# Optimization experiments

Hardware: AMD Instinct MI355X
Metric: run time of the kernel (lower is better)

## Reference

```python
import jax, jax.numpy as jnp
import numpy as np

H, N, CH = 256, 64, 1

def _r2c(x):
    return x[..., 0] + 1j * x[..., 1]

def setup_inputs() -> dict:
    key = jax.random.key(0)
    kA, kB, kC, kdt = jax.random.split(key, 4)
    # Build a Hurwitz A (skew-Hermitian - 0.5*I) so dA = (I-dt/2 A)^-1 (I+dt/2 A) has spectral radius < 1
    M = jax.random.normal(kA, (H, N, N, 2), dtype=jnp.float32) / np.float32(np.sqrt(N))
    Mc = _r2c(M)
    Ac = 0.5 * (Mc - jnp.conjugate(jnp.swapaxes(Mc, -1, -2))) - 0.5 * jnp.eye(N, dtype=Mc.dtype)
    A = jnp.stack([Ac.real, Ac.imag], axis=-1)  # (H,N,N,2)
    B = jax.random.normal(kB, (H, N, 2), dtype=jnp.float32)
    C = jax.random.normal(kC, (CH, H, N, 2), dtype=jnp.float32)
    # log_dt uniform in [log(1e-3), log(1e-1)], shape (H,1) per bilinear docstring
    log_dt = jax.random.uniform(kdt, (H, 1), dtype=jnp.float32,
                                minval=np.float32(np.log(1e-3)), maxval=np.float32(np.log(1e-1)))
    return {"A": A, "B": B, "C": C, "log_dt": log_dt, "L": 2048}

def _bilinear(dt, Ac, Bc):
    # dt: (H,1), Ac: (H,N,N) complex, Bc: (H,N) complex
    n = Ac.shape[-1]
    I = jnp.eye(n, dtype=Ac.dtype)
    half = (dt.astype(Ac.real.dtype) / 2)[:, None]  # (H,1,1)
    A_back = I - half * Ac
    A_fwd = I + half * Ac
    dB = dt.astype(Ac.dtype) * jnp.linalg.solve(A_back, Bc[..., None])[..., 0]  # (H,N)
    dA = jnp.linalg.solve(A_back, A_fwd)  # (H,N,N)
    return dA, dB

def _krylov(L, dA, dB):
    # x[..., l] = dA^l dB via squaring-doubling, matches S4 krylov math
    x = dB[..., None]  # (H,N,1)
    A_ = dA
    while x.shape[-1] < L:
        x = jnp.concatenate([x, jnp.einsum('hnm,hml->hnl', A_, x)], axis=-1)
        A_ = A_ @ A_
    return x[..., :L]

def reference(A, B, C, log_dt, L):
    Ac, Bc, Cc = _r2c(A), _r2c(B), _r2c(C)
    dt = jnp.exp(log_dt)  # (H,1)
    dA, dB = _bilinear(dt, Ac, Bc)
    x = _krylov(L, dA, dB)  # (H,N,L) complex
    # k[c,h,l] = sum_n C[c,h,n] * (dA^l dB)[h,n]; torch .float() on complex keeps real part
    k = jnp.einsum('chn,hnl->chl', Cc, x).real.astype(jnp.float32)
    return k
```

## Files before the change

### kernel.cpp

```cpp
#include <hip/hip_runtime.h>
#include <math.h>

#define NH   256
#define NN   64
#define LSEQ 2048
#define SDW  68
#define NTH  1024

typedef __attribute__((ext_vector_type(8))) short short8;
typedef __attribute__((ext_vector_type(4))) float float4_t;

#define MFMA(a,b,c) __builtin_amdgcn_mfma_f32_16x16x32_bf16((a),(b),(c),0,0,0)
#define PERM_HI 0x07060302u
#define PERM_LO 0x05040100u

static __device__ __forceinline__ unsigned pack2(float v) {
    unsigned hv = __float_as_uint(v) & 0xffff0000u;
    float lo = v - __uint_as_float(hv);
    return __builtin_amdgcn_perm(hv, __float_as_uint(lo), PERM_HI);
}
static __device__ __forceinline__ float unpack2(unsigned w) {
    return __uint_as_float(w & 0xffff0000u) + __uint_as_float(w << 16);
}

static __device__ __forceinline__ void frag_vals(const unsigned* e, short8& hi, short8& lo) {
    unsigned lb[8];
#pragma unroll
    for (int m = 0; m < 8; ++m) {
        unsigned hv = e[m] & 0xffff0000u;
        lb[m] = __float_as_uint(__uint_as_float(e[m]) - __uint_as_float(hv));
    }
    union { short8 s; unsigned u[4]; } H, L;
#pragma unroll
    for (int m = 0; m < 4; ++m) {
        H.u[m] = __builtin_amdgcn_perm(e[2*m+1],  e[2*m],  PERM_HI);
        L.u[m] = __builtin_amdgcn_perm(lb[2*m+1], lb[2*m], PERM_HI);
    }
    hi = H.s; lo = L.s;
}
static __device__ __forceinline__ void frag_f32(const float* p, short8& hi, short8& lo) {
    const uint4* q = (const uint4*)p;
    uint4 d0 = q[0], d1 = q[1];
    unsigned e[8] = {d0.x, d0.y, d0.z, d0.w, d1.x, d1.y, d1.z, d1.w};
    frag_vals(e, hi, lo);
}
static __device__ __forceinline__ void frag_packed(const unsigned* p, short8& hi, short8& lo) {
    const uint4* q = (const uint4*)p;
    uint4 d0 = q[0], d1 = q[1];
    unsigned e[8] = {d0.x, d0.y, d0.z, d0.w, d1.x, d1.y, d1.z, d1.w};
    union { short8 s; unsigned u[4]; } H, L;
#pragma unroll
    for (int m = 0; m < 4; ++m) {
        H.u[m] = __builtin_amdgcn_perm(e[2*m+1], e[2*m], PERM_HI);
        L.u[m] = __builtin_amdgcn_perm(e[2*m+1], e[2*m], PERM_LO);
    }
    hi = H.s; lo = L.s;
}
static __device__ __forceinline__ short8 neg8(short8 v) {
    union { short8 s; int i[4]; } u; u.s = v;
#pragma unroll
    for (int m = 0; m < 4; ++m) u.i[m] ^= 0x80008000;
    return u.s;
}

template<bool AP, bool BP, bool IMAG>
static __device__ __forceinline__ void cmm_tile(
    const void* Ar_, const void* Ai_, const void* Br_, const void* Bi_,
    int arow, int bcol, int fq, float4_t& accR, float4_t& accI)
{
#pragma unroll
    for (int ks = 0; ks < 2; ++ks) {
        const int k0 = ks*32 + fq*8;
        short8 Arh, Arl, Aih, Ail, Brh, Brl, Bih, Bil;
        if (AP) {
            frag_packed((const unsigned*)Ar_ + arow*SDW + k0, Arh, Arl);
            frag_packed((const unsigned*)Ai_ + arow*SDW + k0, Aih, Ail);
        } else {
            frag_f32((const float*)Ar_ + arow*SDW + k0, Arh, Arl);
            frag_f32((const float*)Ai_ + arow*SDW + k0, Aih, Ail);
        }
        if (BP) {
            frag_packed((const unsigned*)Br_ + bcol*SDW + k0, Brh, Brl);
            frag_packed((const unsigned*)Bi_ + bcol*SDW + k0, Bih, Bil);
        } else {
            frag_f32((const float*)Br_ + bcol*SDW + k0, Brh, Brl);
            frag_f32((const float*)Bi_ + bcol*SDW + k0, Bih, Bil);
        }
        short8 nAih = neg8(Aih), nAil = neg8(Ail);
        accR = MFMA(Arh, Brh, accR); accR = MFMA(Arh, Brl, accR); accR = MFMA(Arl, Brh, accR);
        accR = MFMA(nAih, Bih, accR); accR = MFMA(nAih, Bil, accR); accR = MFMA(nAil, Bih, accR);
        if (IMAG) {
            accI = MFMA(Arh, Bih, accI); accI = MFMA(Arh, Bil, accI); accI = MFMA(Arl, Bih, accI);
            accI = MFMA(Aih, Brh, accI); accI = MFMA(Aih, Brl, accI); accI = MFMA(Ail, Brh, accI);
        }
    }
}

__global__ __launch_bounds__(NTH, 4) void ssm_kernel(
    const float* __restrict__ Ag,
    const float* __restrict__ Bg,
    const float* __restrict__ Cg,
    const float* __restrict__ LogDt,
    float* __restrict__ outp)
{
    __shared__ __align__(16) unsigned char lds[130688];
    unsigned* XRr = (unsigned*)(lds +      0);
    unsigned* XRi = (unsigned*)(lds +  17408);
    unsigned* XTr = (unsigned*)(lds +  34816);
    unsigned* XTi = (unsigned*)(lds +  52224);
    float*    Xfr = (float*)(lds +  69632);
    float*    Xfi = (float*)(lds +  87040);
    unsigned* U0u = (unsigned*)Xfr;
    unsigned* U1u = (unsigned*)Xfi;
    float*    Grf = (float*)(lds + 104448);
    float*    Gif = (float*)(lds + 113152);
    float*    Kof = (float*)(lds + 121856);
    float*    bvr = (float*)(lds + 130176);
    float*    bvi = (float*)(lds + 130432);

    const int t    = threadIdx.x;
    const int lane = t & 63;
    const int wv   = t >> 6;
    const int ti   = wv >> 2, tj = wv & 3;
    const int fm   = lane & 15, fq = lane >> 4;
    const int h    = blockIdx.x;

    const float dt  = expf(LogDt[h]);
    const float hdt = 0.5f * dt;

    const float2* A2 = (const float2*)(Ag + (size_t)h * NN * NN * 2);

#pragma unroll
    for (int e = 0; e < 4; ++e) {
        int idx = t + e*NTH;
        int i = idx >> 6, j = idx & 63;
        float2 a = A2[idx];
        unsigned pr = pack2((i == j ? 1.0f : 0.0f) + hdt * a.x);
        unsigned pi = pack2(hdt * a.y);
        XRr[i*SDW + j] = pr; XRi[i*SDW + j] = pi;
        XTr[j*SDW + i] = pr; XTi[j*SDW + i] = pi;
    }
    if (t < NN) {
        float2 bv = ((const float2*)Bg)[h*NN + t];
        float2 cv = ((const float2*)Cg)[h*NN + t];
        bvr[t] = bv.x; bvi[t] = bv.y;
        Grf[t] = cv.x; Gif[t] = cv.y;
    }
    __syncthreads();

    const int arow = ti*16 + fm;
    const int bcol = tj*16 + fm;

#pragma unroll 1
    for (int step = 0; step < 2; ++step) {
        float4_t aR = {0,0,0,0}, aI = {0,0,0,0};
#pragma unroll
        for (int ks = 0; ks < 2; ++ks) {
            const int k0 = ks*32 + fq*8;
            unsigned vr[8], vi[8];
#pragma unroll
            for (int j = 0; j < 8; ++j) {
                float2 a = A2[arow*NN + k0 + j];
                vr[j] = __float_as_uint((arow == k0 + j ? 1.0f : 0.0f) - hdt * a.x);
                vi[j] = __float_as_uint(-hdt * a.y);
            }
            short8 Arh, Arl, Aih, Ail, Brh, Brl, Bih, Bil;
            frag_vals(vr, Arh, Arl);
            frag_vals(vi, Aih, Ail);
            frag_packed(XTr + bcol*SDW + k0, Brh, Brl);
            frag_packed(XTi + bcol*SDW + k0, Bih, Bil);
            short8 nAih = neg8(Aih), nAil = neg8(Ail);
            aR = MFMA(Arh, Brh, aR); aR = MFMA(Arh, Brl, aR); aR = MFMA(Arl, Brh, aR);
            aR = MFMA(nAih, Bih, aR); aR = MFMA(nAih, Bil, aR); aR = MFMA(nAil, Bih, aR);
            aI = MFMA(Arh, Bih, aI); aI = MFMA(Arh, Bil, aI); aI = MFMA(Arl, Bih, aI);
            aI = MFMA(Aih, Brh, aI); aI = MFMA(Aih, Brl, aI); aI = MFMA(Ail, Brh, aI);
        }
#pragma unroll
        for (int r = 0; r < 4; ++r) {
            int row = ti*16 + fq*4 + r;
            U0u[bcol*SDW + row] = pack2((row == bcol ? 2.0f : 0.0f) - aR[r]);
            U1u[bcol*SDW + row] = pack2(-aI[r]);
        }
        __syncthreads();
        float4_t bR = {0,0,0,0}, bI = {0,0,0,0};
        cmm_tile<true, true, true>(XRr, XRi, U0u, U1u, arow, bcol, fq, bR, bI);
        __syncthreads();
#pragma unroll
        for (int r = 0; r < 4; ++r) {
            int row = ti*16 + fq*4 + r;
            unsigned pr = pack2(bR[r]), pi = pack2(bI[r]);
            XRr[row*SDW + bcol] = pr; XRi[row*SDW + bcol] = pi;
            XTr[bcol*SDW + row] = pr; XTi[bcol*SDW + row] = pi;
        }
        __syncthreads();
    }

    {
        int n = t >> 4, part = t & 15;
        float ar = 0.f, ai = 0.f;
#pragma unroll
        for (int qq = 0; qq < 4; ++qq) {
            int k = part + 16*qq;
            float mr = unpack2(XRr[n*SDW + k]), mi = unpack2(XRi[n*SDW + k]);
            ar += mr*bvr[k] - mi*bvi[k];
            ai += mr*bvi[k] + mi*bvr[k];
        }
#pragma unroll
        for (int off = 8; off; off >>= 1) { ar += __shfl_xor(ar, off); ai += __shfl_xor(ai, off); }
        if (part == 0) { Xfr[n] = dt*ar; Xfi[n] = dt*ai; }
    }
    __syncthreads();

#pragma unroll
    for (int e = 0; e < 4; ++e) {
        int idx = t + e*NTH;
        int i = idx >> 6, j = idx & 63;
        float vr = 2.0f*unpack2(XRr[i*SDW + j]) - (i == j ? 1.0f : 0.0f);
        float vi = 2.0f*unpack2(XRi[i*SDW + j]);
        unsigned pr = pack2(vr), pi = pack2(vi);
        XRr[i*SDW + j] = pr; XRi[i*SDW + j] = pi;
        XTr[j*SDW + i] = pr; XTi[j*SDW + i] = pi;
    }
    __syncthreads();

#pragma unroll 1
    for (int s = 1; s <= 11; ++s) {
        if (s <= 6) {
            const int C = 1 << (s-1);
            const int nT = (s == 6) ? 8 : 4;
            if (wv < nT) {
                const int rt = wv >> 2, ct = wv & 3;
                float4_t aR = {0,0,0,0}, aI = {0,0,0,0};
                cmm_tile<false, true, true>(Xfr, Xfi, XRr, XRi, rt*16 + fm, ct*16 + fm, fq, aR, aI);
#pragma unroll
                for (int r = 0; r < 4; ++r) {
                    int row = rt*16 + fq*4 + r;
                    Xfr[(C+row)*SDW + ct*16 + fm] = aR[r];
                    Xfi[(C+row)*SDW + ct*16 + fm] = aI[r];
                }
            }
        } else {
            const int C = 1 << (s-7);
            if (wv < 4) {
                float4_t aR = {0,0,0,0}, aI = {0,0,0,0};
                cmm_tile<false, true, true>(Grf, Gif, XTr, XTi, fm, wv*16 + fm, fq, aR, aI);
#pragma unroll
                for (int r = 0; r < 4; ++r) {
                    int row = fq*4 + r;
                    Grf[(C+row)*SDW + wv*16 + fm] = aR[r];
                    Gif[(C+row)*SDW + wv*16 + fm] = aI[r];
                }
            } else if (s == 11 && wv < 8) {
                int jo = wv - 4;
                float4_t aR = {0,0,0,0}, dummy = {0,0,0,0};
                cmm_tile<false, false, false>(Grf, Gif, Xfr, Xfi, fm, jo*16 + fm, fq, aR, dummy);
#pragma unroll
                for (int r = 0; r < 4; ++r)
                    Kof[(fq*4 + r)*65 + jo*16 + fm] = aR[r];
            }
        }
        if (s <= 10) {
            float4_t sR = {0,0,0,0}, sI = {0,0,0,0};
            cmm_tile<true, true, true>(XRr, XRi, XTr, XTi, arow, bcol, fq, sR, sI);
            __syncthreads();
#pragma unroll
            for (int r = 0; r < 4; ++r) {
                int row = ti*16 + fq*4 + r;
                unsigned pr = pack2(sR[r]), pi = pack2(sI[r]);
                XRr[row*SDW + bcol] = pr; XRi[row*SDW + bcol] = pi;
                XTr[bcol*SDW + row] = pr; XTi[bcol*SDW + row] = pi;
            }
            __syncthreads();
        } else {
            __syncthreads();
        }
    }

    if (wv < 4) {
        float4_t aR = {0,0,0,0}, dummy = {0,0,0,0};
        cmm_tile<false, false, false>(Grf, Gif, Xfr, Xfi, 16 + fm, wv*16 + fm, fq, aR, dummy);
#pragma unroll
        for (int r = 0; r < 4; ++r)
            Kof[(16 + fq*4 + r)*65 + wv*16 + fm] = aR[r];
    }
    __syncthreads();

    {
        int row = t >> 5, col = (t & 31) * 2;
        float2 v = { Kof[row*65 + col], Kof[row*65 + col + 1] };
        ((float2*)(outp + (size_t)h * LSEQ))[t] = v;
    }
}

extern "C" void kernel_launch(void* const* d_in, const int* in_sizes, int n_in,
                              void* d_out, int out_size, void* d_ws, size_t ws_size,
                              hipStream_t stream) {
    const float* A  = (const float*)d_in[0];
    const float* B  = (const float*)d_in[1];
    const float* C  = (const float*)d_in[2];
    const float* ld = (const float*)d_in[3];
    float* out = (float*)d_out;
    ssm_kernel<<<dim3(NH), dim3(NTH), 0, stream>>>(A, B, C, ld, out);
}
```

Measured before the change: 102.1 us.

## Halve block size and register-block complex matmuls into 2x2 tiles per wave

```diff
diff --git a/kernel.cpp b/kernel.cpp
--- a/kernel.cpp
+++ b/kernel.cpp
@@ -5,7 +5,7 @@
 #define NN   64
 #define LSEQ 2048
 #define SDW  68
-#define NTH  1024
+#define NTH  512
 
 typedef __attribute__((ext_vector_type(8))) short short8;
 typedef __attribute__((ext_vector_type(4))) float float4_t;
@@ -63,40 +63,61 @@
     return u.s;
 }
 
-template<bool AP, bool BP, bool IMAG>
-static __device__ __forceinline__ void cmm_tile(
+template<int AG, bool AP, bool BP, bool IMAG>
+static __device__ __forceinline__ void cmm_block(
     const void* Ar_, const void* Ai_, const void* Br_, const void* Bi_,
-    int arow, int bcol, int fq, float4_t& accR, float4_t& accI)
+    int arow0, int bcol0, int fm, int fq,
+    float4_t (&accR)[AG][2], float4_t (&accI)[AG][2])
 {
 #pragma unroll
     for (int ks = 0; ks < 2; ++ks) {
         const int k0 = ks*32 + fq*8;
-        short8 Arh, Arl, Aih, Ail, Brh, Brl, Bih, Bil;
-        if (AP) {
-            frag_packed((const unsigned*)Ar_ + arow*SDW + k0, Arh, Arl);
-            frag_packed((const unsigned*)Ai_ + arow*SDW + k0, Aih, Ail);
-        } else {
-            frag_f32((const float*)Ar_ + arow*SDW + k0, Arh, Arl);
-            frag_f32((const float*)Ai_ + arow*SDW + k0, Aih, Ail);
-        }
-        if (BP) {
-            frag_packed((const unsigned*)Br_ + bcol*SDW + k0, Brh, Brl);
-            frag_packed((const unsigned*)Bi_ + bcol*SDW + k0, Bih, Bil);
-        } else {
-            frag_f32((const float*)Br_ + bcol*SDW + k0, Brh, Brl);
-            frag_f32((const float*)Bi_ + bcol*SDW + k0, Bih, Bil);
-        }
-        short8 nAih = neg8(Aih), nAil = neg8(Ail);
-        accR = MFMA(Arh, Brh, accR); accR = MFMA(Arh, Brl, accR); accR = MFMA(Arl, Brh, accR);
-        accR = MFMA(nAih, Bih, accR); accR = MFMA(nAih, Bil, accR); accR = MFMA(nAil, Bih, accR);
-        if (IMAG) {
-            accI = MFMA(Arh, Bih, accI); accI = MFMA(Arh, Bil, accI); accI = MFMA(Arl, Bih, accI);
-            accI = MFMA(Aih, Brh, accI); accI = MFMA(Aih, Brl, accI); accI = MFMA(Ail, Brh, accI);
-        }
-    }
-}
-
-__global__ __launch_bounds__(NTH, 4) void ssm_kernel(
+        short8 Arh[AG], Arl[AG], Aih[AG], Ail[AG];
+#pragma unroll
+        for (int g = 0; g < AG; ++g) {
+            const int row = arow0 + g*16 + fm;
+            if (AP) {
+                frag_packed((const unsigned*)Ar_ + row*SDW + k0, Arh[g], Arl[g]);
+                frag_packed((const unsigned*)Ai_ + row*SDW + k0, Aih[g], Ail[g]);
+            } else {
+                frag_f32((const float*)Ar_ + row*SDW + k0, Arh[g], Arl[g]);
+                frag_f32((const float*)Ai_ + row*SDW + k0, Aih[g], Ail[g]);
+            }
+        }
+#pragma unroll
+        for (int bg = 0; bg < 2; ++bg) {
+            const int col = bcol0 + bg*16 + fm;
+            short8 Brh, Brl, Bih, Bil;
+            if (BP) {
+                frag_packed((const unsigned*)Br_ + col*SDW + k0, Brh, Brl);
+                frag_packed((const unsigned*)Bi_ + col*SDW + k0, Bih, Bil);
+            } else {
+                frag_f32((const float*)Br_ + col*SDW + k0, Brh, Brl);
+                frag_f32((const float*)Bi_ + col*SDW + k0, Bih, Bil);
+            }
+            short8 nBih = neg8(Bih), nBil = neg8(Bil);
+#pragma unroll
+            for (int g = 0; g < AG; ++g) {
+                accR[g][bg] = MFMA(Arh[g], Brh,  accR[g][bg]);
+                accR[g][bg] = MFMA(Arh[g], Brl,  accR[g][bg]);
+                accR[g][bg] = MFMA(Arl[g], Brh,  accR[g][bg]);
+                accR[g][bg] = MFMA(Aih[g], nBih, accR[g][bg]);
+                accR[g][bg] = MFMA(Aih[g], nBil, accR[g][bg]);
+                accR[g][bg] = MFMA(Ail[g], nBih, accR[g][bg]);
+                if (IMAG) {
+                    accI[g][bg] = MFMA(Arh[g], Bih, accI[g][bg]);
+                    accI[g][bg] = MFMA(Arh[g], Bil, accI[g][bg]);
+                    accI[g][bg] = MFMA(Arl[g], Bih, accI[g][bg]);
+                    accI[g][bg] = MFMA(Aih[g], Brh, accI[g][bg]);
+                    accI[g][bg] = MFMA(Aih[g], Brl, accI[g][bg]);
+                    accI[g][bg] = MFMA(Ail[g], Brh, accI[g][bg]);
+                }
+            }
+        }
+    }
+}
+
+__global__ __launch_bounds__(NTH) void ssm_kernel(
     const float* __restrict__ Ag,
     const float* __restrict__ Bg,
     const float* __restrict__ Cg,
@@ -121,7 +142,6 @@
     const int t    = threadIdx.x;
     const int lane = t & 63;
     const int wv   = t >> 6;
-    const int ti   = wv >> 2, tj = wv & 3;
     const int fm   = lane & 15, fq = lane >> 4;
     const int h    = blockIdx.x;
 
@@ -129,9 +149,10 @@
     const float hdt = 0.5f * dt;
 
     const float2* A2 = (const float2*)(Ag + (size_t)h * NN * NN * 2);
-
-#pragma unroll
-    for (int e = 0; e < 4; ++e) {
+    const float4_t z4 = {0.f, 0.f, 0.f, 0.f};
+
+#pragma unroll
+    for (int e = 0; e < 8; ++e) {
         int idx = t + e*NTH;
         int i = idx >> 6, j = idx & 63;
         float2 a = A2[idx];
@@ -148,71 +169,95 @@
     }
     __syncthreads();
 
-    const int arow = ti*16 + fm;
-    const int bcol = tj*16 + fm;
-
 #pragma unroll 1
     for (int step = 0; step < 2; ++step) {
-        float4_t aR = {0,0,0,0}, aI = {0,0,0,0};
-#pragma unroll
-        for (int ks = 0; ks < 2; ++ks) {
-            const int k0 = ks*32 + fq*8;
-            unsigned vr[8], vi[8];
-#pragma unroll
-            for (int j = 0; j < 8; ++j) {
-                float2 a = A2[arow*NN + k0 + j];
-                vr[j] = __float_as_uint((arow == k0 + j ? 1.0f : 0.0f) - hdt * a.x);
-                vi[j] = __float_as_uint(-hdt * a.y);
-            }
-            short8 Arh, Arl, Aih, Ail, Brh, Brl, Bih, Bil;
-            frag_vals(vr, Arh, Arl);
-            frag_vals(vi, Aih, Ail);
-            frag_packed(XTr + bcol*SDW + k0, Brh, Brl);
-            frag_packed(XTi + bcol*SDW + k0, Bih, Bil);
-            short8 nAih = neg8(Aih), nAil = neg8(Ail);
-            aR = MFMA(Arh, Brh, aR); aR = MFMA(Arh, Brl, aR); aR = MFMA(Arl, Brh, aR);
-            aR = MFMA(nAih, Bih, aR); aR = MFMA(nAih, Bil, aR); aR = MFMA(nAil, Bih, aR);
-            aI = MFMA(Arh, Bih, aI); aI = MFMA(Arh, Bil, aI); aI = MFMA(Arl, Bih, aI);
-            aI = MFMA(Aih, Brh, aI); aI = MFMA(Aih, Brl, aI); aI = MFMA(Ail, Brh, aI);
-        }
-#pragma unroll
-        for (int r = 0; r < 4; ++r) {
-            int row = ti*16 + fq*4 + r;
-            U0u[bcol*SDW + row] = pack2((row == bcol ? 2.0f : 0.0f) - aR[r]);
-            U1u[bcol*SDW + row] = pack2(-aI[r]);
-        }
-        __syncthreads();
-        float4_t bR = {0,0,0,0}, bI = {0,0,0,0};
-        cmm_tile<true, true, true>(XRr, XRi, U0u, U1u, arow, bcol, fq, bR, bI);
-        __syncthreads();
-#pragma unroll
-        for (int r = 0; r < 4; ++r) {
-            int row = ti*16 + fq*4 + r;
-            unsigned pr = pack2(bR[r]), pi = pack2(bI[r]);
-            XRr[row*SDW + bcol] = pr; XRi[row*SDW + bcol] = pi;
-            XTr[bcol*SDW + row] = pr; XTi[bcol*SDW + row] = pi;
+        {
+            const int arow0 = (wv >> 1) * 16;
+            const int bcol0 = (wv & 1) * 32;
+            float4_t aR[2], aI[2];
+            aR[0] = z4; aR[1] = z4; aI[0] = z4; aI[1] = z4;
+#pragma unroll
+            for (int ks = 0; ks < 2; ++ks) {
+                const int k0 = ks*32 + fq*8;
+                const int row = arow0 + fm;
+                unsigned vr[8], vi[8];
+#pragma unroll
+                for (int j = 0; j < 8; ++j) {
+                    float2 a = A2[row*NN + k0 + j];
+                    vr[j] = __float_as_uint((row == k0 + j ? 1.0f : 0.0f) - hdt * a.x);
+                    vi[j] = __float_as_uint(-hdt * a.y);
+                }
+                short8 Arh, Arl, Aih, Ail;
+                frag_vals(vr, Arh, Arl);
+                frag_vals(vi, Aih, Ail);
+#pragma unroll
+                for (int bg = 0; bg < 2; ++bg) {
+                    const int col = bcol0 + bg*16 + fm;
+                    short8 Brh, Brl, Bih, Bil;
+                    frag_packed(XTr + col*SDW + k0, Brh, Brl);
+                    frag_packed(XTi + col*SDW + k0, Bih, Bil);
+                    short8 nBih = neg8(Bih), nBil = neg8(Bil);
+                    aR[bg] = MFMA(Arh, Brh,  aR[bg]); aR[bg] = MFMA(Arh, Brl,  aR[bg]);
+                    aR[bg] = MFMA(Arl, Brh,  aR[bg]); aR[bg] = MFMA(Aih, nBih, aR[bg]);
+                    aR[bg] = MFMA(Aih, nBil, aR[bg]); aR[bg] = MFMA(Ail, nBih, aR[bg]);
+                    aI[bg] = MFMA(Arh, Bih,  aI[bg]); aI[bg] = MFMA(Arh, Bil,  aI[bg]);
+                    aI[bg] = MFMA(Arl, Bih,  aI[bg]); aI[bg] = MFMA(Aih, Brh,  aI[bg]);
+                    aI[bg] = MFMA(Aih, Brl,  aI[bg]); aI[bg] = MFMA(Ail, Brh,  aI[bg]);
+                }
+            }
+#pragma unroll
+            for (int bg = 0; bg < 2; ++bg)
+#pragma unroll
+                for (int r = 0; r < 4; ++r) {
+                    int row = arow0 + fq*4 + r;
+                    int col = bcol0 + bg*16 + fm;
+                    U0u[col*SDW + row] = pack2((row == col ? 2.0f : 0.0f) - aR[bg][r]);
+                    U1u[col*SDW + row] = pack2(-aI[bg][r]);
+                }
+        }
+        __syncthreads();
+        float4_t bR[2][2], bI[2][2];
+        bR[0][0]=z4; bR[0][1]=z4; bR[1][0]=z4; bR[1][1]=z4;
+        bI[0][0]=z4; bI[0][1]=z4; bI[1][0]=z4; bI[1][1]=z4;
+        if (wv < 4)
+            cmm_block<2, true, true, true>(XRr, XRi, U0u, U1u,
+                                           (wv>>1)*32, (wv&1)*32, fm, fq, bR, bI);
+        __syncthreads();
+        if (wv < 4) {
+#pragma unroll
+            for (int g = 0; g < 2; ++g)
+#pragma unroll
+                for (int bg = 0; bg < 2; ++bg)
+#pragma unroll
+                    for (int r = 0; r < 4; ++r) {
+                        int row = (wv>>1)*32 + g*16 + fq*4 + r;
+                        int col = (wv&1)*32 + bg*16 + fm;
+                        unsigned pr = pack2(bR[g][bg][r]), pi = pack2(bI[g][bg][r]);
+                        XRr[row*SDW + col] = pr; XRi[row*SDW + col] = pi;
+                        XTr[col*SDW + row] = pr; XTi[col*SDW + row] = pi;
+                    }
         }
         __syncthreads();
     }
 
     {
-        int n = t >> 4, part = t & 15;
+        int n = t >> 3, part = t & 7;
         float ar = 0.f, ai = 0.f;
 #pragma unroll
-        for (int qq = 0; qq < 4; ++qq) {
-            int k = part + 16*qq;
+        for (int qq = 0; qq < 8; ++qq) {
+            int k = part + 8*qq;
             float mr = unpack2(XRr[n*SDW + k]), mi = unpack2(XRi[n*SDW + k]);
             ar += mr*bvr[k] - mi*bvi[k];
             ai += mr*bvi[k] + mi*bvr[k];
         }
 #pragma unroll
-        for (int off = 8; off; off >>= 1) { ar += __shfl_xor(ar, off); ai += __shfl_xor(ai, off); }
+        for (int off = 4; off; off >>= 1) { ar += __shfl_xor(ar, off); ai += __shfl_xor(ai, off); }
         if (part == 0) { Xfr[n] = dt*ar; Xfi[n] = dt*ai; }
     }
     __syncthreads();
 
 #pragma unroll
-    for (int e = 0; e < 4; ++e) {
+    for (int e = 0; e < 8; ++e) {
         int idx = t + e*NTH;
         int i = idx >> 6, j = idx & 63;
         float vr = 2.0f*unpack2(XRr[i*SDW + j]) - (i == j ? 1.0f : 0.0f);
@@ -225,70 +270,116 @@
 
 #pragma unroll 1
     for (int s = 1; s <= 11; ++s) {
+        const bool dosq = (s <= 10);
+        float4_t sR[2][2], sI[2][2];
+        sR[0][0]=z4; sR[0][1]=z4; sR[1][0]=z4; sR[1][1]=z4;
+        sI[0][0]=z4; sI[0][1]=z4; sI[1][0]=z4; sI[1][1]=z4;
+        if (wv < 4 && dosq)
+            cmm_block<2, true, true, true>(XRr, XRi, XTr, XTi,
+                                           (wv>>1)*32, (wv&1)*32, fm, fq, sR, sI);
+        float4_t p1R[1][2], p1I[1][2];
+        p1R[0][0]=z4; p1R[0][1]=z4; p1I[0][0]=z4; p1I[0][1]=z4;
+        float4_t p2R[2][2], p2I[2][2];
+        p2R[0][0]=z4; p2R[0][1]=z4; p2R[1][0]=z4; p2R[1][1]=z4;
+        p2I[0][0]=z4; p2I[0][1]=z4; p2I[1][0]=z4; p2I[1][1]=z4;
+        int C;
         if (s <= 6) {
-            const int C = 1 << (s-1);
-            const int nT = (s == 6) ? 8 : 4;
-            if (wv < nT) {
-                const int rt = wv >> 2, ct = wv & 3;
-                float4_t aR = {0,0,0,0}, aI = {0,0,0,0};
-                cmm_tile<false, true, true>(Xfr, Xfi, XRr, XRi, rt*16 + fm, ct*16 + fm, fq, aR, aI);
-#pragma unroll
-                for (int r = 0; r < 4; ++r) {
-                    int row = rt*16 + fq*4 + r;
-                    Xfr[(C+row)*SDW + ct*16 + fm] = aR[r];
-                    Xfi[(C+row)*SDW + ct*16 + fm] = aI[r];
-                }
+            C = 1 << (s-1);
+            if (wv == 4 || wv == 5) {
+                if (s == 6)
+                    cmm_block<2, false, true, true>(Xfr, Xfi, XRr, XRi,
+                                                    0, (wv-4)*32, fm, fq, p2R, p2I);
+                else
+                    cmm_block<1, false, true, true>(Xfr, Xfi, XRr, XRi,
+                                                    0, (wv-4)*32, fm, fq, p1R, p1I);
             }
         } else {
-            const int C = 1 << (s-7);
-            if (wv < 4) {
-                float4_t aR = {0,0,0,0}, aI = {0,0,0,0};
-                cmm_tile<false, true, true>(Grf, Gif, XTr, XTi, fm, wv*16 + fm, fq, aR, aI);
-#pragma unroll
-                for (int r = 0; r < 4; ++r) {
-                    int row = fq*4 + r;
-                    Grf[(C+row)*SDW + wv*16 + fm] = aR[r];
-                    Gif[(C+row)*SDW + wv*16 + fm] = aI[r];
-                }
-            } else if (s == 11 && wv < 8) {
-                int jo = wv - 4;
-                float4_t aR = {0,0,0,0}, dummy = {0,0,0,0};
-                cmm_tile<false, false, false>(Grf, Gif, Xfr, Xfi, fm, jo*16 + fm, fq, aR, dummy);
+            C = 1 << (s-7);
+            if (wv == 4 || wv == 5)
+                cmm_block<1, false, true, true>(Grf, Gif, XTr, XTi,
+                                                0, (wv-4)*32, fm, fq, p1R, p1I);
+            if (s == 11 && (wv == 6 || wv == 7))
+                cmm_block<1, false, false, false>(Grf, Gif, Xfr, Xfi,
+                                                  0, (wv-6)*32, fm, fq, p1R, p1I);
+        }
+        if (wv == 4 || wv == 5) {
+            const int cb = (wv-4)*32;
+            if (s == 6) {
+#pragma unroll
+                for (int g = 0; g < 2; ++g)
+#pragma unroll
+                    for (int bg = 0; bg < 2; ++bg)
+#pragma unroll
+                        for (int r = 0; r < 4; ++r) {
+                            int row = 32 + g*16 + fq*4 + r;
+                            int col = cb + bg*16 + fm;
+                            Xfr[row*SDW + col] = p2R[g][bg][r];
+                            Xfi[row*SDW + col] = p2I[g][bg][r];
+                        }
+            } else if (s <= 5) {
+#pragma unroll
+                for (int bg = 0; bg < 2; ++bg)
+#pragma unroll
+                    for (int r = 0; r < 4; ++r) {
+                        int row = C + fq*4 + r;
+                        int col = cb + bg*16 + fm;
+                        Xfr[row*SDW + col] = p1R[0][bg][r];
+                        Xfi[row*SDW + col] = p1I[0][bg][r];
+                    }
+            } else {
+#pragma unroll
+                for (int bg = 0; bg < 2; ++bg)
+#pragma unroll
+                    for (int r = 0; r < 4; ++r) {
+                        int row = C + fq*4 + r;
+                        int col = cb + bg*16 + fm;
+                        Grf[row*SDW + col] = p1R[0][bg][r];
+                        Gif[row*SDW + col] = p1I[0][bg][r];
+                    }
+            }
+        }
+        if (s == 11 && (wv == 6 || wv == 7)) {
+#pragma unroll
+            for (int bg = 0; bg < 2; ++bg)
 #pragma unroll
                 for (int r = 0; r < 4; ++r)
-                    Kof[(fq*4 + r)*65 + jo*16 + fm] = aR[r];
-            }
-        }
-        if (s <= 10) {
-            float4_t sR = {0,0,0,0}, sI = {0,0,0,0};
-            cmm_tile<true, true, true>(XRr, XRi, XTr, XTi, arow, bcol, fq, sR, sI);
-            __syncthreads();
-#pragma unroll
-            for (int r = 0; r < 4; ++r) {
-                int row = ti*16 + fq*4 + r;
-                unsigned pr = pack2(sR[r]), pi = pack2(sI[r]);
-                XRr[row*SDW + bcol] = pr; XRi[row*SDW + bcol] = pi;
-                XTr[bcol*SDW + row] = pr; XTi[bcol*SDW + row] = pi;
-            }
-            __syncthreads();
-        } else {
-            __syncthreads();
-        }
-    }
-
-    if (wv < 4) {
-        float4_t aR = {0,0,0,0}, dummy = {0,0,0,0};
-        cmm_tile<false, false, false>(Grf, Gif, Xfr, Xfi, 16 + fm, wv*16 + fm, fq, aR, dummy);
-#pragma unroll
-        for (int r = 0; r < 4; ++r)
-            Kof[(16 + fq*4 + r)*65 + wv*16 + fm] = aR[r];
+                    Kof[(fq*4 + r)*65 + (wv-6)*32 + bg*16 + fm] = p1R[0][bg][r];
+        }
+        __syncthreads();
+        if (wv < 4 && dosq) {
+#pragma unroll
+            for (int g = 0; g < 2; ++g)
+#pragma unroll
+                for (int bg = 0; bg < 2; ++bg)
+#pragma unroll
+                    for (int r = 0; r < 4; ++r) {
+                        int row = (wv>>1)*32 + g*16 + fq*4 + r;
+                        int col = (wv&1)*32 + bg*16 + fm;
+                        unsigned pr = pack2(sR[g][bg][r]), pi = pack2(sI[g][bg][r]);
+                        XRr[row*SDW + col] = pr; XRi[row*SDW + col] = pi;
+                        XTr[col*SDW + row] = pr; XTi[col*SDW + row] = pi;
+                    }
+        }
+        __syncthreads();
+    }
+
+    if (wv < 2) {
+        float4_t kR[1][2], kI[1][2];
+        kR[0][0]=z4; kR[0][1]=z4; kI[0][0]=z4; kI[0][1]=z4;
+        cmm_block<1, false, false, false>(Grf, Gif, Xfr, Xfi, 16, wv*32, fm, fq, kR, kI);
+#pragma unroll
+        for (int bg = 0; bg < 2; ++bg)
+#pragma unroll
+            for (int r = 0; r < 4; ++r)
+                Kof[(16 + fq*4 + r)*65 + wv*32 + bg*16 + fm] = kR[0][bg][r];
     }
     __syncthreads();
 
     {
-        int row = t >> 5, col = (t & 31) * 2;
-        float2 v = { Kof[row*65 + col], Kof[row*65 + col + 1] };
-        ((float2*)(outp + (size_t)h * LSEQ))[t] = v;
+        int row = t >> 4, col = (t & 15) * 4;
+        const float4_t* src = (const float4_t*)(Kof + row*65 + col);
+        float4_t v = *src;
+        ((float4*)(outp + (size_t)h * LSEQ))[t] = make_float4(v[0], v[1], v[2], v[3]);
     }
 }
 
```

Result: slower. 105.6 us (+3.5%).

## Replace resolvent Newton steps with polynomial iteration and shorten squaring chain

Applied to the files above, without the earlier changes.

```diff
diff --git a/kernel.cpp b/kernel.cpp
--- a/kernel.cpp
+++ b/kernel.cpp
@@ -129,6 +129,7 @@
     const float hdt = 0.5f * dt;
 
     const float2* A2 = (const float2*)(Ag + (size_t)h * NN * NN * 2);
+    const float4_t z4 = {0.f, 0.f, 0.f, 0.f};
 
 #pragma unroll
     for (int e = 0; e < 4; ++e) {
@@ -151,9 +152,8 @@
     const int arow = ti*16 + fm;
     const int bcol = tj*16 + fm;
 
-#pragma unroll 1
-    for (int step = 0; step < 2; ++step) {
-        float4_t aR = {0,0,0,0}, aI = {0,0,0,0};
+    {
+        float4_t aR = z4, aI = z4;
 #pragma unroll
         for (int ks = 0; ks < 2; ++ks) {
             const int k0 = ks*32 + fq*8;
@@ -176,24 +176,62 @@
             aI = MFMA(Aih, Brh, aI); aI = MFMA(Aih, Brl, aI); aI = MFMA(Ail, Brh, aI);
         }
 #pragma unroll
+        for (int rp = 0; rp < 2; ++rp) {
+            int row0 = ti*16 + fq*4 + rp*2;
+            uint2 wr; wr.x = pack2(aR[rp*2]); wr.y = pack2(aR[rp*2+1]);
+            uint2 wi; wi.x = pack2(aI[rp*2]); wi.y = pack2(aI[rp*2+1]);
+            *(uint2*)(U0u + bcol*SDW + row0) = wr;
+            *(uint2*)(U1u + bcol*SDW + row0) = wi;
+        }
+    }
+    __syncthreads();
+
+    {
+        float4_t aR = z4, aI = z4;
+        cmm_tile<true, true, true>(XRr, XRi, U0u, U1u, arow, bcol, fq, aR, aI);
+        __syncthreads();
+#pragma unroll
         for (int r = 0; r < 4; ++r) {
             int row = ti*16 + fq*4 + r;
-            U0u[bcol*SDW + row] = pack2((row == bcol ? 2.0f : 0.0f) - aR[r]);
-            U1u[bcol*SDW + row] = pack2(-aI[r]);
-        }
-        __syncthreads();
-        float4_t bR = {0,0,0,0}, bI = {0,0,0,0};
-        cmm_tile<true, true, true>(XRr, XRi, U0u, U1u, arow, bcol, fq, bR, bI);
-        __syncthreads();
+            XRr[row*SDW + bcol] = pack2(aR[r]);
+            XRi[row*SDW + bcol] = pack2(aI[r]);
+        }
+    }
+    __syncthreads();
+
+    {
+        float4_t aR = z4, aI = z4;
+        cmm_tile<true, true, true>(XRr, XRi, U0u, U1u, arow, bcol, fq, aR, aI);
+        float o_r[4], o_i[4];
 #pragma unroll
         for (int r = 0; r < 4; ++r) {
             int row = ti*16 + fq*4 + r;
-            unsigned pr = pack2(bR[r]), pi = pack2(bI[r]);
-            XRr[row*SDW + bcol] = pr; XRi[row*SDW + bcol] = pi;
-            XTr[bcol*SDW + row] = pr; XTi[bcol*SDW + row] = pi;
-        }
-        __syncthreads();
-    }
+            float2 a = A2[row*NN + bcol];
+            float x1r = (row == bcol ? 1.0f : 0.0f) + hdt * a.x;
+            float x1i = hdt * a.y;
+            float vvr = unpack2(XRr[row*SDW + bcol]);
+            float vvi = unpack2(XRi[row*SDW + bcol]);
+            o_r[r] = 3.0f*x1r - 3.0f*vvr + aR[r];
+            o_i[r] = 3.0f*x1i - 3.0f*vvi + aI[r];
+        }
+        __syncthreads();
+        unsigned pr[4], pi[4];
+#pragma unroll
+        for (int r = 0; r < 4; ++r) {
+            int row = ti*16 + fq*4 + r;
+            pr[r] = pack2(o_r[r]); pi[r] = pack2(o_i[r]);
+            XRr[row*SDW + bcol] = pr[r]; XRi[row*SDW + bcol] = pi[r];
+        }
+#pragma unroll
+        for (int rp = 0; rp < 2; ++rp) {
+            int row0 = ti*16 + fq*4 + rp*2;
+            uint2 wr; wr.x = pr[rp*2]; wr.y = pr[rp*2+1];
+            uint2 wi; wi.x = pi[rp*2]; wi.y = pi[rp*2+1];
+            *(uint2*)(XTr + bcol*SDW + row0) = wr;
+            *(uint2*)(XTi + bcol*SDW + row0) = wi;
+        }
+    }
+    __syncthreads();
 
     {
         int n = t >> 4, part = t & 15;
@@ -224,13 +262,13 @@
     __syncthreads();
 
 #pragma unroll 1
-    for (int s = 1; s <= 11; ++s) {
+    for (int s = 1; s <= 9; ++s) {
         if (s <= 6) {
             const int C = 1 << (s-1);
             const int nT = (s == 6) ? 8 : 4;
             if (wv < nT) {
                 const int rt = wv >> 2, ct = wv & 3;
-                float4_t aR = {0,0,0,0}, aI = {0,0,0,0};
+                float4_t aR = z4, aI = z4;
                 cmm_tile<false, true, true>(Xfr, Xfi, XRr, XRi, rt*16 + fm, ct*16 + fm, fq, aR, aI);
 #pragma unroll
                 for (int r = 0; r < 4; ++r) {
@@ -242,7 +280,7 @@
         } else {
             const int C = 1 << (s-7);
             if (wv < 4) {
-                float4_t aR = {0,0,0,0}, aI = {0,0,0,0};
+                float4_t aR = z4, aI = z4;
                 cmm_tile<false, true, true>(Grf, Gif, XTr, XTi, fm, wv*16 + fm, fq, aR, aI);
 #pragma unroll
                 for (int r = 0; r < 4; ++r) {
@@ -250,40 +288,56 @@
                     Grf[(C+row)*SDW + wv*16 + fm] = aR[r];
                     Gif[(C+row)*SDW + wv*16 + fm] = aI[r];
                 }
-            } else if (s == 11 && wv < 8) {
-                int jo = wv - 4;
-                float4_t aR = {0,0,0,0}, dummy = {0,0,0,0};
-                cmm_tile<false, false, false>(Grf, Gif, Xfr, Xfi, fm, jo*16 + fm, fq, aR, dummy);
+            }
+        }
+        float4_t sR = z4, sI = z4;
+        cmm_tile<true, true, true>(XRr, XRi, XTr, XTi, arow, bcol, fq, sR, sI);
+        __syncthreads();
+        unsigned pr[4], pi[4];
+#pragma unroll
+        for (int r = 0; r < 4; ++r) {
+            int row = ti*16 + fq*4 + r;
+            pr[r] = pack2(sR[r]); pi[r] = pack2(sI[r]);
+            XRr[row*SDW + bcol] = pr[r]; XRi[row*SDW + bcol] = pi[r];
+        }
+#pragma unroll
+        for (int rp = 0; rp < 2; ++rp) {
+            int row0 = ti*16 + fq*4 + rp*2;
+            uint2 wr; wr.x = pr[rp*2]; wr.y = pr[rp*2+1];
+            uint2 wi; wi.x = pi[rp*2]; wi.y = pi[rp*2+1];
+            *(uint2*)(XTr + bcol*SDW + row0) = wr;
+            *(uint2*)(XTi + bcol*SDW + row0) = wi;
+        }
+        __syncthreads();
+    }
+
+#pragma unroll 1
+    for (int tt = 0; tt < 4; ++tt) {
+        if (tt < 3 && wv < 4) {
+            const int ab = tt * 8;
+            float4_t aR = z4, aI = z4;
+            cmm_tile<false, true, true>(Grf, Gif, XTr, XTi, ab + fm, wv*16 + fm, fq, aR, aI);
+#pragma unroll
+            for (int r = 0; r < 4; ++r) {
+                int orow = 8 + ab + fq*4 + r;
+                if (orow < 32) {
+                    Grf[orow*SDW + wv*16 + fm] = aR[r];
+                    Gif[orow*SDW + wv*16 + fm] = aI[r];
+                }
+            }
+        }
+        if (wv >= 4 && wv < 8) {
+            const int jb = tt * 8;
+            float4_t aR = z4, aI = z4;
+            cmm_tile<false, false, false>(Grf, Gif, Xfr, Xfi, jb + fm, (wv-4)*16 + fm, fq, aR, aI);
+            if (fq < 2) {
 #pragma unroll
                 for (int r = 0; r < 4; ++r)
-                    Kof[(fq*4 + r)*65 + jo*16 + fm] = aR[r];
-            }
-        }
-        if (s <= 10) {
-            float4_t sR = {0,0,0,0}, sI = {0,0,0,0};
-            cmm_tile<true, true, true>(XRr, XRi, XTr, XTi, arow, bcol, fq, sR, sI);
-            __syncthreads();
-#pragma unroll
-            for (int r = 0; r < 4; ++r) {
-                int row = ti*16 + fq*4 + r;
-                unsigned pr = pack2(sR[r]), pi = pack2(sI[r]);
-                XRr[row*SDW + bcol] = pr; XRi[row*SDW + bcol] = pi;
-                XTr[bcol*SDW + row] = pr; XTi[bcol*SDW + row] = pi;
-            }
-            __syncthreads();
-        } else {
-            __syncthreads();
-        }
-    }
-
-    if (wv < 4) {
-        float4_t aR = {0,0,0,0}, dummy = {0,0,0,0};
-        cmm_tile<false, false, false>(Grf, Gif, Xfr, Xfi, 16 + fm, wv*16 + fm, fq, aR, dummy);
-#pragma unroll
-        for (int r = 0; r < 4; ++r)
-            Kof[(16 + fq*4 + r)*65 + wv*16 + fm] = aR[r];
-    }
-    __syncthreads();
+                    Kof[(jb + fq*4 + r)*65 + (wv-4)*16 + fm] = aR[r];
+            }
+        }
+        __syncthreads();
+    }
 
     {
         int row = t >> 5, col = (t & 31) * 2;
```

New measurement: 97.18 us. 4.8% less time.
